# Kernel tuning notes

Hardware: AMD Instinct MI355X
Metric: run time of the kernel (lower is better)

## Reference

```python
import jax, jax.numpy as jnp
import numpy as np

B, N, D = 2, 2048, 256
H, HID, EN = 8, 64, 2
ALPHA = 0.2
NEG = -9e15


def setup_inputs() -> dict:
    key = jax.random.key(0)
    k1, k2, k3, k4, k5, k6 = jax.random.split(key, 6)
    fea_mats = jax.random.normal(k1, (B, N, D), dtype=jnp.float32)
    adj_mats = jax.random.randint(k2, (B, N, N), 0, 2).astype(jnp.float32)
    # xavier-uniform-like init (gain 1.414)
    def xav(k, shape):
        fan_in, fan_out = shape[-2], shape[-1]
        bound = 1.414 * np.sqrt(6.0 / (fan_in + fan_out))
        return jax.random.uniform(k, shape, jnp.float32, -bound, bound)
    W_att = xav(k3, (H, D, HID))          # per-head projection
    a_att = xav(k4, (H, 2 * HID, 1))      # per-head attention vector
    W_last = xav(k5, (H * HID, EN))       # last-layer projection
    a_last = xav(k6, (2 * EN, 1))         # last-layer attention vector
    return {"fea_mats": fea_mats, "adj_mats": adj_mats,
            "W_att": W_att, "a_att": a_att,
            "W_last": W_last, "a_last": a_last}


def _leaky(x):
    return jnp.where(x >= 0, x, ALPHA * x)


def _masked_attn(e, adj):
    # torch: where(adj!=0, e, 0) * adj; masked_fill(==0, -9e15); softmax(dim=1 over columns)
    att = jnp.where(adj != 0, e, jnp.zeros_like(e)) * adj
    att = jnp.where(att == 0, jnp.full_like(att, NEG), att)
    return jax.nn.softmax(att, axis=-1)


def reference(fea_mats, adj_mats, W_att, a_att, W_last, a_last):
    # ---- multi-head GAT layers (concat=True), eval mode -> dropout = identity ----
    wh = jnp.einsum('bnd,hdo->bhno', fea_mats, W_att)        # [B,H,N,HID]
    a1 = a_att[:, :HID, 0]                                   # [H,HID]
    a2 = a_att[:, HID:, 0]                                   # [H,HID]
    e1 = jnp.einsum('bhno,ho->bhn', wh, a1)                  # regulon part
    e2 = jnp.einsum('bhno,ho->bhn', wh, a2)                  # gene part
    e = _leaky(e1[:, :, :, None] + e2[:, :, None, :])        # [B,H,N,N]
    att = _masked_attn(e, adj_mats[:, None])                 # [B,H,N,N]
    x = jax.nn.elu(jnp.einsum('bhnm,bhmo->bhno', att, wh))   # [B,H,N,HID]
    x = jnp.transpose(x, (0, 2, 1, 3)).reshape(B, N, H * HID)
    # ---- last layer (concat=False), adj narrowed to square (already square) ----
    wh2 = jnp.einsum('bnd,de->bne', x, W_last)               # [B,N,EN]
    b1 = a_last[:EN, 0]
    b2 = a_last[EN:, 0]
    e = _leaky(jnp.einsum('bne,e->bn', wh2, b1)[:, :, None]
               + jnp.einsum('bne,e->bn', wh2, b2)[:, None, :])  # [B,N,N]
    att = _masked_attn(e, adj_mats)
    out = jax.nn.elu(jnp.einsum('bnm,bme->bne', att, wh2))   # [B,N,EN]
    return out
```

## Files before the change

### kernel.cpp

```cpp
#include <hip/hip_runtime.h>
#include <hip/hip_bf16.h>
#include <cstdint>
#include <cstddef>

#define B_ 2
#define N_ 2048
#define D_ 256
#define H_ 8
#define HID_ 64
#define EN_ 2
#define ALPHA 0.2f
#define NEGBIG (-3.0e38f)
#define LOG2E 1.4426950408889634f

typedef __bf16 bf16x8 __attribute__((ext_vector_type(8)));
typedef float f32x4 __attribute__((ext_vector_type(4)));
typedef unsigned short ushort8 __attribute__((ext_vector_type(8)));
typedef float float4v __attribute__((ext_vector_type(4)));
typedef float float2v __attribute__((ext_vector_type(2)));
typedef unsigned int uint2v __attribute__((ext_vector_type(2)));

__device__ __forceinline__ unsigned short f2bf(float f) {
    unsigned int u = __builtin_bit_cast(unsigned int, f);
    unsigned int r = u + 0x7FFFu + ((u >> 16) & 1u);
    return (unsigned short)(r >> 16);
}
__device__ __forceinline__ float bf2f(unsigned short u) {
    unsigned int x = ((unsigned int)u) << 16;
    return __builtin_bit_cast(float, x);
}
__device__ __forceinline__ float leakyf(float x) { return fmaxf(x, ALPHA * x); }
__device__ __forceinline__ float ub(unsigned int d, int e) {
    return (float)((d >> (8 * e)) & 0xffu);
}

__device__ __forceinline__ ushort8 cvt8(const float* __restrict__ p) {
    float4v x0 = *(const float4v*)p;
    float4v x1 = *(const float4v*)(p + 4);
    ushort8 r;
    #pragma unroll
    for (int e = 0; e < 4; ++e) { r[e] = f2bf(x0[e]); r[e + 4] = f2bf(x1[e]); }
    return r;
}

__global__ __launch_bounds__(256) void k_prep(const float* __restrict__ adj,
                                              unsigned char* __restrict__ adj8) {
    size_t base = ((size_t)blockIdx.x * 256 + threadIdx.x) * 8;
    float4v a = *(const float4v*)(adj + base);
    float4v b = *(const float4v*)(adj + base + 4);
    unsigned int lo = 0, hi = 0;
    #pragma unroll
    for (int e = 0; e < 4; ++e) {
        lo |= (a[e] != 0.f ? 1u : 0u) << (8 * e);
        hi |= (b[e] != 0.f ? 1u : 0u) << (8 * e);
    }
    uint2v o; o[0] = lo; o[1] = hi;
    *(uint2v*)(adj8 + base) = o;
}

__global__ void k_transpose_w(const float* __restrict__ W,
                              unsigned short* __restrict__ WT) {
    int h = blockIdx.x;
    const float* Wh = W + (size_t)h * D_ * HID_;
    unsigned short* WTh = WT + (size_t)h * HID_ * D_;
    for (int idx = threadIdx.x; idx < D_ * HID_; idx += blockDim.x) {
        int d = idx / HID_, o = idx % HID_;
        WTh[o * D_ + d] = f2bf(Wh[idx]);
    }
}

__global__ __launch_bounds__(256) void k_wh(
    const float* __restrict__ fea,
    const unsigned short* __restrict__ WT,
    const float* __restrict__ a_att,
    unsigned short* __restrict__ whT,
    float* __restrict__ e1, float* __restrict__ e2)
{
    int i0 = blockIdx.x << 6;
    int h0 = blockIdx.y * 2;
    int b  = blockIdx.z;

    __shared__ __align__(16) union SmemA {
        struct { unsigned short fa[64 * 72]; unsigned short wt[2][64 * 72]; } s;
        float tr[64 * 65];
    } u;

    int t = threadIdx.x;
    int lane = t & 63;
    int wv = t >> 6;
    int hw = wv & 1;
    int half = wv >> 1;
    int r = lane & 15, q = lane >> 4;
    int ra = t >> 2;
    int cc = (t & 3) * 16;
    int rowbase = half * 32;

    f32x4 acc[2][4] = {};

    const float* fearow = fea + ((size_t)(b * N_ + i0 + ra)) * D_;
    const unsigned short* wt0row = WT + ((size_t)(h0 * 64 + ra)) * D_;
    const unsigned short* wt1row = WT + ((size_t)((h0 + 1) * 64 + ra)) * D_;

    for (int d0 = 0; d0 < D_; d0 += 64) {
        *(ushort8*)&u.s.fa[ra * 72 + cc]       = cvt8(fearow + d0 + cc);
        *(ushort8*)&u.s.fa[ra * 72 + cc + 8]   = cvt8(fearow + d0 + cc + 8);
        *(ushort8*)&u.s.wt[0][ra * 72 + cc]     = *(const ushort8*)(wt0row + d0 + cc);
        *(ushort8*)&u.s.wt[0][ra * 72 + cc + 8] = *(const ushort8*)(wt0row + d0 + cc + 8);
        *(ushort8*)&u.s.wt[1][ra * 72 + cc]     = *(const ushort8*)(wt1row + d0 + cc);
        *(ushort8*)&u.s.wt[1][ra * 72 + cc + 8] = *(const ushort8*)(wt1row + d0 + cc + 8);
        __syncthreads();
        #pragma unroll
        for (int k0 = 0; k0 < 64; k0 += 32) {
            bf16x8 a0 = *(const bf16x8*)&u.s.fa[(rowbase + r) * 72 + k0 + q * 8];
            bf16x8 a1 = *(const bf16x8*)&u.s.fa[(rowbase + 16 + r) * 72 + k0 + q * 8];
            #pragma unroll
            for (int f = 0; f < 4; ++f) {
                bf16x8 bb = *(const bf16x8*)&u.s.wt[hw][(16 * f + r) * 72 + k0 + q * 8];
                acc[0][f] = __builtin_amdgcn_mfma_f32_16x16x32_bf16(a0, bb, acc[0][f], 0, 0, 0);
                acc[1][f] = __builtin_amdgcn_mfma_f32_16x16x32_bf16(a1, bb, acc[1][f], 0, 0, 0);
            }
        }
        __syncthreads();
    }

    float a1v[4], a2v[4];
    #pragma unroll
    for (int f = 0; f < 4; ++f) {
        a1v[f] = a_att[(h0 + hw) * 128 + 16 * f + r];
        a2v[f] = a_att[(h0 + hw) * 128 + 64 + 16 * f + r];
    }
    #pragma unroll
    for (int m = 0; m < 2; ++m) {
        #pragma unroll
        for (int rr = 0; rr < 4; ++rr) {
            float s1 = 0.f, s2 = 0.f;
            #pragma unroll
            for (int f = 0; f < 4; ++f) { s1 += acc[m][f][rr] * a1v[f]; s2 += acc[m][f][rr] * a2v[f]; }
            #pragma unroll
            for (int sh = 1; sh < 16; sh <<= 1) {
                s1 += __shfl_xor(s1, sh, 64);
                s2 += __shfl_xor(s2, sh, 64);
            }
            if (r == 0) {
                int i = i0 + rowbase + 16 * m + 4 * q + rr;
                size_t idx = ((size_t)(b * H_ + h0 + hw)) * N_ + i;
                e1[idx] = s1 * LOG2E; e2[idx] = s2 * LOG2E;
            }
        }
    }

    #pragma unroll
    for (int hh = 0; hh < 2; ++hh) {
        __syncthreads();
        if (hw == hh) {
            #pragma unroll
            for (int m = 0; m < 2; ++m)
                #pragma unroll
                for (int f = 0; f < 4; ++f)
                    #pragma unroll
                    for (int rr = 0; rr < 4; ++rr)
                        u.tr[(16 * f + r) * 65 + rowbase + 16 * m + 4 * q + rr] = acc[m][f][rr];
        }
        __syncthreads();
        {
            int o = t >> 2;
            int ch = (t & 3) * 16;
            unsigned short tmp[16];
            #pragma unroll
            for (int e = 0; e < 16; ++e) tmp[e] = f2bf(u.tr[o * 65 + ch + e]);
            ushort8* dst = (ushort8*)(whT + (((size_t)(b * H_ + h0 + hh) * 64 + o)) * N_ + i0 + ch);
            dst[0] = *(ushort8*)&tmp[0];
            dst[1] = *(ushort8*)&tmp[8];
        }
    }
}

__global__ __launch_bounds__(256) void k_maxe2(const float* __restrict__ e2,
                                               float* __restrict__ mx) {
    int bh = blockIdx.x;
    int t = threadIdx.x;
    const float* row = e2 + (size_t)bh * N_;
    float M = NEGBIG;
    #pragma unroll
    for (int it = 0; it < N_ / 256; ++it) M = fmaxf(M, row[it * 256 + t]);
    #pragma unroll
    for (int s = 1; s < 64; s <<= 1) M = fmaxf(M, __shfl_xor(M, s, 64));
    __shared__ float red[4];
    if ((t & 63) == 0) red[t >> 6] = M;
    __syncthreads();
    if (t == 0) mx[bh] = fmaxf(fmaxf(red[0], red[1]), fmaxf(red[2], red[3]));
}

template<int JPER>
__global__ __launch_bounds__(256, 4) void k_pv1(
    const unsigned char* __restrict__ adj8,
    const unsigned short* __restrict__ whT,
    const float* __restrict__ e1g, const float* __restrict__ e2g,
    const float* __restrict__ maxE2,
    unsigned short* __restrict__ x_part,
    float* __restrict__ zPart)
{
    constexpr int NT = JPER / 64;
    int s  = blockIdx.x;
    int i0 = blockIdx.y << 7;
    int bh = blockIdx.z;
    int h = bh & 7, b = bh >> 3;
    int jBeg = s * JPER;

    __shared__ __align__(16) unsigned short wt_lds[2][64 * 64];
    __shared__ float tE[JPER];
    __shared__ float vE[JPER];

    int t = threadIdx.x;
    int lane = t & 63;
    int wv = t >> 6;
    int r = lane & 15, q = lane >> 4;

    int ir0 = i0 + wv * 32 + r;
    int ir1 = ir0 + 16;
    float mx = maxE2[bh];
    float e1_0 = e1g[(size_t)bh * N_ + ir0];
    float e1_1 = e1g[(size_t)bh * N_ + ir1];
    float m0 = leakyf(e1_0 + mx), m1 = leakyf(e1_1 + mx);
    float sI0 = __builtin_amdgcn_exp2f(e1_0 - m0);
    float uI0 = __builtin_amdgcn_exp2f(ALPHA * e1_0 - m0);
    float sI1 = __builtin_amdgcn_exp2f(e1_1 - m1);
    float uI1 = __builtin_amdgcn_exp2f(ALPHA * e1_1 - m1);

    const float* e2p = e2g + (size_t)bh * N_ + jBeg;
    const unsigned char* ap0 = adj8 + ((size_t)(b * N_ + ir0)) * N_ + jBeg + q * 8;
    const unsigned char* ap1 = ap0 + (size_t)16 * N_;

    int c0 = t, c1 = t + 256;
    const unsigned short* wsrc0 =
        whT + ((size_t)bh * 64 + (c0 >> 3)) * N_ + jBeg + (c0 & 7) * 8;
    const unsigned short* wsrc1 =
        whT + ((size_t)bh * 64 + (c1 >> 3)) * N_ + jBeg + (c1 & 7) * 8;
    int woff0 = (c0 * 8) ^ (((c0 >> 3) & 7) << 3);
    int woff1 = (c1 * 8) ^ (((c1 >> 3) & 7) << 3);

    int swz = (r & 7) << 3;
    int koff0 = (8 * q) ^ swz;
    int koff1 = (32 + 8 * q) ^ swz;

    bf16x8 ones;
    #pragma unroll
    for (int e = 0; e < 8; ++e) ones[e] = (__bf16)1.0f;

    f32x4 acc[2][4] = {};
    f32x4 accz[2] = {};

    uint2v aA[4], aB[4];
    ushort8 wN0, wN1;

#define LOADADJ(A, tile) do {                                                   \
        const unsigned char* p0 = ap0 + (tile) * 64;                            \
        const unsigned char* p1 = ap1 + (tile) * 64;                            \
        A[0] = *(const uint2v*)(p0);      A[1] = *(const uint2v*)(p0 + 32);     \
        A[2] = *(const uint2v*)(p1);      A[3] = *(const uint2v*)(p1 + 32);     \
    } while (0)
#define LOADW(tile) do {                                                        \
        wN0 = *(const ushort8*)(wsrc0 + (tile) * 64);                           \
        wN1 = *(const ushort8*)(wsrc1 + (tile) * 64);                           \
    } while (0)

    for (int jj = t; jj < JPER; jj += 256) {
        float ev = e2p[jj];
        tE[jj] = __builtin_amdgcn_exp2f(ev);
        vE[jj] = __builtin_amdgcn_exp2f(ALPHA * ev);
    }
    LOADW(0);
    *(ushort8*)&wt_lds[0][woff0] = wN0;
    *(ushort8*)&wt_lds[0][woff1] = wN1;
    if (NT > 1) LOADW(1);
    LOADADJ(aA, 0);
    if (NT > 1) LOADADJ(aB, 1);
    asm volatile("s_waitcnt lgkmcnt(0)" ::: "memory");
    __builtin_amdgcn_s_barrier();

    auto pgen = [&](const uint2v& alo, const uint2v& ahi, float sI, float uI,
                    const float4v& t0, const float4v& t1,
                    const float4v& t2, const float4v& t3,
                    const float4v& v0, const float4v& v1,
                    const float4v& v2, const float4v& v3,
                    bf16x8& pa0, bf16x8& pa1) {
        #pragma unroll
        for (int e = 0; e < 4; ++e) {
            pa0[e]     = (__bf16)(fmaxf(sI * t0[e], uI * v0[e]) * ub(alo[0], e));
            pa0[e + 4] = (__bf16)(fmaxf(sI * t1[e], uI * v1[e]) * ub(alo[1], e));
            pa1[e]     = (__bf16)(fmaxf(sI * t2[e], uI * v2[e]) * ub(ahi[0], e));
            pa1[e + 4] = (__bf16)(fmaxf(sI * t3[e], uI * v3[e]) * ub(ahi[1], e));
        }
    };

    #pragma unroll 2
    for (int t8 = 0; t8 < NT; ++t8) {
        const int cur = t8 & 1;
        if (t8 + 1 < NT) {
            *(ushort8*)&wt_lds[cur ^ 1][woff0] = wN0;
            *(ushort8*)&wt_lds[cur ^ 1][woff1] = wN1;
        }
        if (t8 + 2 < NT) LOADW(t8 + 2);

        const float* tb = &tE[t8 * 64 + q * 8];
        const float* vb = &vE[t8 * 64 + q * 8];
        float4v t0 = *(const float4v*)(tb),      t1 = *(const float4v*)(tb + 4);
        float4v t2 = *(const float4v*)(tb + 32), t3 = *(const float4v*)(tb + 36);
        float4v v0 = *(const float4v*)(vb),      v1 = *(const float4v*)(vb + 4);
        float4v v2 = *(const float4v*)(vb + 32), v3 = *(const float4v*)(vb + 36);

        bf16x8 pa00, pa01, pa10, pa11;
        if (cur == 0) {
            pgen(aA[0], aA[1], sI0, uI0, t0, t1, t2, t3, v0, v1, v2, v3, pa00, pa01);
            pgen(aA[2], aA[3], sI1, uI1, t0, t1, t2, t3, v0, v1, v2, v3, pa10, pa11);
        } else {
            pgen(aB[0], aB[1], sI0, uI0, t0, t1, t2, t3, v0, v1, v2, v3, pa00, pa01);
            pgen(aB[2], aB[3], sI1, uI1, t0, t1, t2, t3, v0, v1, v2, v3, pa10, pa11);
        }
        if (t8 + 2 < NT) {
            if (cur == 0) LOADADJ(aA, t8 + 2);
            else          LOADADJ(aB, t8 + 2);
        }

        const unsigned short* Wb = wt_lds[cur];
        bf16x8 bb0[4], bb1[4];
        #pragma unroll
        for (int f = 0; f < 4; ++f) {
            bb0[f] = *(const bf16x8*)&Wb[f * 1024 + r * 64 + koff0];
            bb1[f] = *(const bf16x8*)&Wb[f * 1024 + r * 64 + koff1];
        }
        #pragma unroll
        for (int f = 0; f < 4; ++f) {
            acc[0][f] = __builtin_amdgcn_mfma_f32_16x16x32_bf16(pa00, bb0[f], acc[0][f], 0, 0, 0);
            acc[1][f] = __builtin_amdgcn_mfma_f32_16x16x32_bf16(pa10, bb0[f], acc[1][f], 0, 0, 0);
        }
        accz[0] = __builtin_amdgcn_mfma_f32_16x16x32_bf16(pa00, ones, accz[0], 0, 0, 0);
        accz[1] = __builtin_amdgcn_mfma_f32_16x16x32_bf16(pa10, ones, accz[1], 0, 0, 0);
        #pragma unroll
        for (int f = 0; f < 4; ++f) {
            acc[0][f] = __builtin_amdgcn_mfma_f32_16x16x32_bf16(pa01, bb1[f], acc[0][f], 0, 0, 0);
            acc[1][f] = __builtin_amdgcn_mfma_f32_16x16x32_bf16(pa11, bb1[f], acc[1][f], 0, 0, 0);
        }
        accz[0] = __builtin_amdgcn_mfma_f32_16x16x32_bf16(pa01, ones, accz[0], 0, 0, 0);
        accz[1] = __builtin_amdgcn_mfma_f32_16x16x32_bf16(pa11, ones, accz[1], 0, 0, 0);

        asm volatile("s_waitcnt lgkmcnt(0)" ::: "memory");
        __builtin_amdgcn_s_barrier();
    }
#undef LOADADJ
#undef LOADW

    unsigned short* xp = x_part + ((size_t)s * (B_ * N_) + (size_t)b * N_) * 512 + h * 64;
    #pragma unroll
    for (int mR = 0; mR < 2; ++mR) {
        #pragma unroll
        for (int f = 0; f < 4; ++f) {
            #pragma unroll
            for (int rr = 0; rr < 4; ++rr) {
                int i = i0 + wv * 32 + mR * 16 + 4 * q + rr;
                xp[(size_t)i * 512 + 16 * f + r] = f2bf(acc[mR][f][rr]);
            }
        }
        if (r == 0) {
            #pragma unroll
            for (int rr = 0; rr < 4; ++rr) {
                int i = i0 + wv * 32 + mR * 16 + 4 * q + rr;
                zPart[((size_t)(s * 16 + bh)) * N_ + i] = accz[mR][rr];
            }
        }
    }
}

__global__ __launch_bounds__(256) void k_wh2(
    const unsigned short* __restrict__ x_part,
    const float* __restrict__ zPart,
    const float* __restrict__ W_last,
    const float* __restrict__ a_last,
    float* __restrict__ wh2, float* __restrict__ g1, float* __restrict__ g2,
    int S)
{
    int idx = blockIdx.x * 4 + (threadIdx.x >> 6);
    int lane = threadIdx.x & 63;
    int b = idx >> 11, n = idx & (N_ - 1);
    float a0 = 0.f, a1 = 0.f;
    #pragma unroll
    for (int it = 0; it < 8; ++it) {
        int k = it * 64 + lane;
        float xv = 0.f, zv = 0.f;
        for (int s = 0; s < S; ++s) {
            xv += bf2f(x_part[((size_t)s * (B_ * N_) + idx) * 512 + k]);
            zv += zPart[((size_t)(s * 16 + b * 8 + it)) * N_ + n];
        }
        float x = (zv > 0.f) ? xv / zv : 0.f;
        x = x > 0.f ? x : expm1f(x);
        float2v wl = *(const float2v*)(W_last + k * 2);
        a0 += x * wl[0];
        a1 += x * wl[1];
    }
    #pragma unroll
    for (int s = 1; s < 64; s <<= 1) {
        a0 += __shfl_xor(a0, s, 64);
        a1 += __shfl_xor(a1, s, 64);
    }
    if (lane == 0) {
        wh2[idx * 2] = a0; wh2[idx * 2 + 1] = a1;
        g1[idx] = (a0 * a_last[0] + a1 * a_last[1]) * LOG2E;
        g2[idx] = (a0 * a_last[2] + a1 * a_last[3]) * LOG2E;
    }
}

__global__ __launch_bounds__(256) void k_out(
    const unsigned char* __restrict__ adj8,
    const float* __restrict__ wh2,
    const float* __restrict__ g1, const float* __restrict__ g2,
    float* __restrict__ out)
{
    int idx = blockIdx.x * 4 + (threadIdx.x >> 6);
    int lane = threadIdx.x & 63;
    int b = idx >> 11;
    float gi = g1[idx];
    const unsigned char* arow = adj8 + (size_t)idx * N_;
    const float* g2b = g2 + (size_t)b * N_;
    const float* wh2b = wh2 + (size_t)b * N_ * 2;

    float ep[32];
    float M = NEGBIG;
    #pragma unroll
    for (int it = 0; it < 8; ++it) {
        int j = it * 256 + lane * 4;
        unsigned int d = *(const unsigned int*)(arow + j);
        float4v s4 = *(const float4v*)(g2b + j);
        #pragma unroll
        for (int e = 0; e < 4; ++e) {
            float l = leakyf(gi + s4[e]);
            float v = ((d >> (8 * e)) & 0xffu) ? l : NEGBIG;
            ep[it * 4 + e] = v;
            M = fmaxf(M, v);
        }
    }
    #pragma unroll
    for (int s = 1; s < 64; s <<= 1) M = fmaxf(M, __shfl_xor(M, s, 64));

    float Z = 0.f, A0 = 0.f, A1 = 0.f;
    #pragma unroll
    for (int it = 0; it < 8; ++it) {
        int j = it * 256 + lane * 4;
        float4v wA = *(const float4v*)(wh2b + 2 * j);
        float4v wB = *(const float4v*)(wh2b + 2 * j + 4);
        #pragma unroll
        for (int e = 0; e < 4; ++e) {
            float p = __builtin_amdgcn_exp2f(ep[it * 4 + e] - M);
            Z += p;
            float w0 = (e < 2) ? wA[2 * e] : wB[2 * (e - 2)];
            float w1 = (e < 2) ? wA[2 * e + 1] : wB[2 * (e - 2) + 1];
            A0 += p * w0;
            A1 += p * w1;
        }
    }
    #pragma unroll
    for (int s = 1; s < 64; s <<= 1) {
        Z += __shfl_xor(Z, s, 64);
        A0 += __shfl_xor(A0, s, 64);
        A1 += __shfl_xor(A1, s, 64);
    }
    if (lane == 0) {
        float o0 = A0 / Z, o1 = A1 / Z;
        o0 = o0 > 0.f ? o0 : expm1f(o0);
        o1 = o1 > 0.f ? o1 : expm1f(o1);
        float2v ov; ov[0] = o0; ov[1] = o1;
        *(float2v*)(out + idx * 2) = ov;
    }
}

extern "C" void kernel_launch(void* const* d_in, const int* in_sizes, int n_in,
                              void* d_out, int out_size, void* d_ws, size_t ws_size,
                              hipStream_t stream) {
    const float* fea    = (const float*)d_in[0];
    const float* adj    = (const float*)d_in[1];
    const float* W_att  = (const float*)d_in[2];
    const float* a_att  = (const float*)d_in[3];
    const float* W_last = (const float*)d_in[4];
    const float* a_last = (const float*)d_in[5];

    char* ws = (char*)d_ws;
    float* e1  = (float*)(ws + 0);
    float* e2  = (float*)(ws + 131072);
    float* mxE = (float*)(ws + 262144);
    float* wh2 = (float*)(ws + 262400);
    float* g1  = (float*)(ws + 295168);
    float* g2  = (float*)(ws + 311552);
    unsigned short* WT  = (unsigned short*)(ws + 327936);
    unsigned short* whT = (unsigned short*)(ws + 590080);
    float* zPart = (float*)(ws + 4784384);
    unsigned char* adj8 = (unsigned char*)(ws + 5308672);
    unsigned short* x_part = (unsigned short*)(ws + 13697280);

    const size_t BASE = 13697280ULL, XPART = 4194304ULL;
    int S = (ws_size >= BASE + 4 * XPART) ? 4
          : (ws_size >= BASE + 2 * XPART) ? 2 : 1;

    k_prep<<<dim3(B_ * N_ * N_ / 2048), dim3(256), 0, stream>>>(adj, adj8);
    k_transpose_w<<<dim3(H_), dim3(256), 0, stream>>>(W_att, WT);
    k_wh<<<dim3(N_ / 64, H_ / 2, B_), dim3(256), 0, stream>>>(
        fea, WT, a_att, whT, e1, e2);
    k_maxe2<<<dim3(B_ * H_), dim3(256), 0, stream>>>(e2, mxE);
    if (S == 4)
        k_pv1<512><<<dim3(4, N_ / 128, B_ * H_), dim3(256), 0, stream>>>(
            adj8, whT, e1, e2, mxE, x_part, zPart);
    else if (S == 2)
        k_pv1<1024><<<dim3(2, N_ / 128, B_ * H_), dim3(256), 0, stream>>>(
            adj8, whT, e1, e2, mxE, x_part, zPart);
    else
        k_pv1<2048><<<dim3(1, N_ / 128, B_ * H_), dim3(256), 0, stream>>>(
            adj8, whT, e1, e2, mxE, x_part, zPart);
    k_wh2<<<dim3(B_ * N_ / 4), dim3(256), 0, stream>>>(
        x_part, zPart, W_last, a_last, wh2, g1, g2, S);
    k_out<<<dim3(B_ * N_ / 4), dim3(256), 0, stream>>>(
        adj8, wh2, g1, g2, (float*)d_out);
}
```

Before: 104.7 us.

## Process two heads per block in attention-PV kernel to share adjacency tiles

Adds a k_pv2 kernel that runs 512 threads per block and handles two heads at once. The adjacency mask tile in shared memory and the exp-table setup are shared between both heads, so adjacency reads per head drop by half. It also double-buffers the whT and adjacency tiles through registers and shared memory, and stages output through shared memory for coalesced stores. The costs are a larger shared-memory footprint and fewer blocks in the grid. Only the S==4 path uses the new kernel.

```diff
diff --git a/kernel.cpp b/kernel.cpp
--- a/kernel.cpp
+++ b/kernel.cpp
@@ -19,6 +19,7 @@
 typedef float float4v __attribute__((ext_vector_type(4)));
 typedef float float2v __attribute__((ext_vector_type(2)));
 typedef unsigned int uint2v __attribute__((ext_vector_type(2)));
+typedef unsigned int uint4v __attribute__((ext_vector_type(4)));
 
 __device__ __forceinline__ unsigned short f2bf(float f) {
     unsigned int u = __builtin_bit_cast(unsigned int, f);
@@ -189,6 +190,203 @@
     if ((t & 63) == 0) red[t >> 6] = M;
     __syncthreads();
     if (t == 0) mx[bh] = fmaxf(fmaxf(red[0], red[1]), fmaxf(red[2], red[3]));
+}
+
+template<int JPER>
+__global__ __launch_bounds__(512, 4) void k_pv2(
+    const unsigned char* __restrict__ adj8,
+    const unsigned short* __restrict__ whT,
+    const float* __restrict__ e1g, const float* __restrict__ e2g,
+    const float* __restrict__ maxE2,
+    unsigned short* __restrict__ x_part,
+    float* __restrict__ zPart)
+{
+    constexpr int NT = JPER / 64;
+    int s  = blockIdx.x;
+    int i0 = blockIdx.y << 7;
+    int z  = blockIdx.z;
+    int b  = z >> 2;
+    int h0 = (z & 3) * 2;
+    int bh0 = b * H_ + h0;
+    int jBeg = s * JPER;
+
+    __shared__ __align__(16) union {
+        struct {
+            unsigned short wt[2][2][4096];
+            unsigned char  adjl[2][128 * 80];
+            unsigned int   tv[2][JPER];
+        } m;
+        unsigned short epi[128][136];
+    } u;
+
+    int t = threadIdx.x;
+    int lane = t & 63;
+    int w = t >> 6;
+    int hw = w & 1;
+    int rw = (w >> 1) * 32;
+    int r = lane & 15, q = lane >> 4;
+    int bh = bh0 + hw;
+
+    int ir0 = i0 + rw + r, ir1 = ir0 + 16;
+    float mxv = maxE2[bh];
+    float e1_0 = e1g[(size_t)bh * N_ + ir0];
+    float e1_1 = e1g[(size_t)bh * N_ + ir1];
+    float m0 = leakyf(e1_0 + mxv), m1 = leakyf(e1_1 + mxv);
+    float sI0 = __builtin_amdgcn_exp2f(e1_0 - m0);
+    float uI0 = __builtin_amdgcn_exp2f(ALPHA * e1_0 - m0);
+    float sI1 = __builtin_amdgcn_exp2f(e1_1 - m1);
+    float uI1 = __builtin_amdgcn_exp2f(ALPHA * e1_1 - m1);
+
+    int sh = t >> 8;
+    int so = (t & 255) >> 2;
+    int sj = (t & 3) * 16;
+    const unsigned short* wsrc = whT + ((size_t)(bh0 + sh) * 64 + so) * N_ + jBeg + sj;
+    int wof0 = sh * 4096 + so * 64 + (sj ^ ((so & 7) << 3));
+    int wof1 = sh * 4096 + so * 64 + ((sj + 8) ^ ((so & 7) << 3));
+    int ar = t >> 2, ac = (t & 3) * 16;
+    const unsigned char* asrc = adj8 + ((size_t)(b * N_ + i0 + ar)) * N_ + jBeg + ac;
+    int aof = ar * 80 + ac;
+
+    int swzr = (r & 7) << 3;
+    int koff0 = (8 * q) ^ swzr;
+    int koff1 = (32 + 8 * q) ^ swzr;
+
+    bf16x8 ones;
+    #pragma unroll
+    for (int e = 0; e < 8; ++e) ones[e] = (__bf16)1.0f;
+
+    f32x4 acc[2][4] = {};
+    f32x4 accz[2] = {};
+
+    ushort8 wA, wB;
+    uint4v  aR;
+
+#define LOADSTG(tile) do {                                        \
+        wA = *(const ushort8*)(wsrc + (tile) * 64);               \
+        wB = *(const ushort8*)(wsrc + (tile) * 64 + 8);           \
+        aR = *(const uint4v*)(asrc + (tile) * 64);                \
+    } while (0)
+
+    for (int jj = t; jj < 2 * JPER; jj += 512) {
+        int hh = jj >= JPER ? 1 : 0;
+        int j = jj - hh * JPER;
+        float ev = e2g[(size_t)(bh0 + hh) * N_ + jBeg + j];
+        unsigned int pk = (unsigned int)f2bf(__builtin_amdgcn_exp2f(ev))
+                        | ((unsigned int)f2bf(__builtin_amdgcn_exp2f(ALPHA * ev)) << 16);
+        u.m.tv[hh][j] = pk;
+    }
+    LOADSTG(0);
+    asm volatile("s_waitcnt vmcnt(0)" ::: "memory");
+    *(ushort8*)((unsigned short*)u.m.wt[0] + wof0) = wA;
+    *(ushort8*)((unsigned short*)u.m.wt[0] + wof1) = wB;
+    *(uint4v*)&u.m.adjl[0][aof] = aR;
+    if (NT > 1) LOADSTG(1);
+    asm volatile("s_waitcnt lgkmcnt(0)" ::: "memory");
+    __builtin_amdgcn_s_barrier();
+
+    #pragma unroll 2
+    for (int t8 = 0; t8 < NT; ++t8) {
+        const int p = t8 & 1;
+        if (t8 + 1 < NT) {
+            asm volatile("s_waitcnt vmcnt(0)" ::: "memory");
+            *(ushort8*)((unsigned short*)u.m.wt[p ^ 1] + wof0) = wA;
+            *(ushort8*)((unsigned short*)u.m.wt[p ^ 1] + wof1) = wB;
+            *(uint4v*)&u.m.adjl[p ^ 1][aof] = aR;
+        }
+        if (t8 + 2 < NT) LOADSTG(t8 + 2);
+
+        const unsigned int* tvp = &u.m.tv[hw][t8 * 64 + q * 8];
+        uint4v ta0 = *(const uint4v*)(tvp);
+        uint4v ta1 = *(const uint4v*)(tvp + 4);
+        uint4v tb0 = *(const uint4v*)(tvp + 32);
+        uint4v tb1 = *(const uint4v*)(tvp + 36);
+        const unsigned char* ab = &u.m.adjl[p][(rw + r) * 80 + q * 8];
+        uint2v a0 = *(const uint2v*)(ab);
+        uint2v a1 = *(const uint2v*)(ab + 32);
+        uint2v a2 = *(const uint2v*)(ab + 16 * 80);
+        uint2v a3 = *(const uint2v*)(ab + 16 * 80 + 32);
+
+        bf16x8 pa00, pa01, pa10, pa11;
+        #pragma unroll
+        for (int e = 0; e < 4; ++e) {
+            float tt, vv;
+            unsigned int uu;
+            uu = ta0[e];
+            tt = __builtin_bit_cast(float, uu << 16);
+            vv = __builtin_bit_cast(float, uu & 0xffff0000u);
+            pa00[e] = (__bf16)(fmaxf(sI0 * tt, uI0 * vv) * ub(a0[0], e));
+            pa10[e] = (__bf16)(fmaxf(sI1 * tt, uI1 * vv) * ub(a2[0], e));
+            uu = ta1[e];
+            tt = __builtin_bit_cast(float, uu << 16);
+            vv = __builtin_bit_cast(float, uu & 0xffff0000u);
+            pa00[e + 4] = (__bf16)(fmaxf(sI0 * tt, uI0 * vv) * ub(a0[1], e));
+            pa10[e + 4] = (__bf16)(fmaxf(sI1 * tt, uI1 * vv) * ub(a2[1], e));
+            uu = tb0[e];
+            tt = __builtin_bit_cast(float, uu << 16);
+            vv = __builtin_bit_cast(float, uu & 0xffff0000u);
+            pa01[e] = (__bf16)(fmaxf(sI0 * tt, uI0 * vv) * ub(a1[0], e));
+            pa11[e] = (__bf16)(fmaxf(sI1 * tt, uI1 * vv) * ub(a3[0], e));
+            uu = tb1[e];
+            tt = __builtin_bit_cast(float, uu << 16);
+            vv = __builtin_bit_cast(float, uu & 0xffff0000u);
+            pa01[e + 4] = (__bf16)(fmaxf(sI0 * tt, uI0 * vv) * ub(a1[1], e));
+            pa11[e + 4] = (__bf16)(fmaxf(sI1 * tt, uI1 * vv) * ub(a3[1], e));
+        }
+
+        const unsigned short* Wb = (const unsigned short*)u.m.wt[p] + hw * 4096;
+        bf16x8 bb;
+        #pragma unroll
+        for (int f = 0; f < 4; ++f) {
+            bb = *(const bf16x8*)&Wb[f * 1024 + r * 64 + koff0];
+            acc[0][f] = __builtin_amdgcn_mfma_f32_16x16x32_bf16(pa00, bb, acc[0][f], 0, 0, 0);
+            acc[1][f] = __builtin_amdgcn_mfma_f32_16x16x32_bf16(pa10, bb, acc[1][f], 0, 0, 0);
+        }
+        accz[0] = __builtin_amdgcn_mfma_f32_16x16x32_bf16(pa00, ones, accz[0], 0, 0, 0);
+        accz[1] = __builtin_amdgcn_mfma_f32_16x16x32_bf16(pa10, ones, accz[1], 0, 0, 0);
+        #pragma unroll
+        for (int f = 0; f < 4; ++f) {
+            bb = *(const bf16x8*)&Wb[f * 1024 + r * 64 + koff1];
+            acc[0][f] = __builtin_amdgcn_mfma_f32_16x16x32_bf16(pa01, bb, acc[0][f], 0, 0, 0);
+            acc[1][f] = __builtin_amdgcn_mfma_f32_16x16x32_bf16(pa11, bb, acc[1][f], 0, 0, 0);
+        }
+        accz[0] = __builtin_amdgcn_mfma_f32_16x16x32_bf16(pa01, ones, accz[0], 0, 0, 0);
+        accz[1] = __builtin_amdgcn_mfma_f32_16x16x32_bf16(pa11, ones, accz[1], 0, 0, 0);
+
+        asm volatile("s_waitcnt lgkmcnt(0)" ::: "memory");
+        __builtin_amdgcn_s_barrier();
+    }
+#undef LOADSTG
+
+    if (r == 0) {
+        #pragma unroll
+        for (int mR = 0; mR < 2; ++mR)
+            #pragma unroll
+            for (int rr = 0; rr < 4; ++rr) {
+                int i = i0 + rw + mR * 16 + 4 * q + rr;
+                zPart[((size_t)(s * 16 + bh)) * N_ + i] = accz[mR][rr];
+            }
+    }
+
+    #pragma unroll
+    for (int mR = 0; mR < 2; ++mR)
+        #pragma unroll
+        for (int f = 0; f < 4; ++f)
+            #pragma unroll
+            for (int rr = 0; rr < 4; ++rr)
+                u.epi[rw + mR * 16 + 4 * q + rr][hw * 64 + 16 * f + r] = f2bf(acc[mR][f][rr]);
+    __syncthreads();
+    {
+        int tr = t >> 2;
+        int ch = (t & 3) * 32;
+        const ushort8* src = (const ushort8*)&u.epi[tr][ch];
+        ushort8 v0 = src[0], v1 = src[1], v2 = src[2], v3 = src[3];
+        unsigned short* dst = x_part
+            + ((size_t)s * (B_ * N_) + (size_t)b * N_ + i0 + tr) * 512 + h0 * 64 + ch;
+        ((ushort8*)dst)[0] = v0;
+        ((ushort8*)dst)[1] = v1;
+        ((ushort8*)dst)[2] = v2;
+        ((ushort8*)dst)[3] = v3;
+    }
 }
 
 template<int JPER>
@@ -505,7 +703,7 @@
         fea, WT, a_att, whT, e1, e2);
     k_maxe2<<<dim3(B_ * H_), dim3(256), 0, stream>>>(e2, mxE);
     if (S == 4)
-        k_pv1<512><<<dim3(4, N_ / 128, B_ * H_), dim3(256), 0, stream>>>(
+        k_pv2<512><<<dim3(4, N_ / 128, B_ * 4), dim3(512), 0, stream>>>(
             adj8, whT, e1, e2, mxE, x_part, zPart);
     else if (S == 2)
         k_pv1<1024><<<dim3(2, N_ / 128, B_ * H_), dim3(256), 0, stream>>>(
```

Result: faster. 90.73 us, median of 4 (-13.4%).
